# Kernel tuning notes

Hardware: AMD Instinct MI355X
Metric: run time of the kernel (lower is better)

Reference implementation:

```python
import jax, jax.numpy as jnp
import numpy as np

N, F, H, R, E = 50000, 128, 128, 8, 800000
BN_EPS = 1e-5


def setup_inputs() -> dict:
    key = jax.random.key(0)
    ks = jax.random.split(key, 10)
    g = lambda k, shp: jax.random.normal(k, shp, dtype=jnp.float32) * (1.0 / np.sqrt(shp[-2] if len(shp) > 1 else shp[-1]))
    return {
        "x": jax.random.normal(ks[0], (N, F), dtype=jnp.float32),
        "edge_index": jax.random.randint(ks[1], (2, E), 0, N, dtype=jnp.int32),
        "edge_type": jax.random.randint(ks[2], (E,), 0, R, dtype=jnp.int32),
        "W1": g(ks[3], (F, H)),
        "b1": jnp.zeros((H,), jnp.float32),
        "weight": g(ks[4], (R, H, H)),
        "root": g(ks[5], (H, H)),
        "bias_c": jnp.zeros((H,), jnp.float32),
        "gamma": jnp.ones((H,), jnp.float32),
        "beta": jnp.zeros((H,), jnp.float32),
        "W2": g(ks[6], (H, H)),
        "b2": jnp.zeros((H,), jnp.float32),
        "Wo": g(ks[7], (H, 1)),
        "bo": jnp.zeros((1,), jnp.float32),
    }


def reference(x, edge_index, edge_type, W1, b1, weight, root, bias_c, gamma, beta, W2, b2, Wo, bo):
    n = x.shape[0]
    r = weight.shape[0]
    src, dst = edge_index[0], edge_index[1]
    # segment id combining relation and destination node: equivalent to the
    # per-relation edge-mask + scatter-add loop in RGCNConv, but in one pass.
    seg = edge_type.astype(jnp.int32) * n + dst

    def conv(h):
        msg = h[src]                                            # [E, H] gather
        agg = jax.ops.segment_sum(msg, seg, num_segments=r * n)  # [R*N, H]
        agg = agg.reshape(r, n, -1)                             # [R, N, H]
        out = jnp.einsum('rnc,rco->no', agg, weight)            # per-relation matmul, summed
        return out + h @ root + bias_c

    def bn(h):
        mu = h.mean(axis=0)
        var = h.var(axis=0)  # biased var, matches torch BN training normalization
        return gamma * (h - mu) * jax.lax.rsqrt(var + BN_EPS) + beta

    h = x @ W1 + b1
    h = jax.nn.relu(bn(conv(h)))
    h = jax.nn.relu(bn(conv(h)))
    h = h @ W2 + b2
    h = h @ Wo + bo
    return jax.nn.sigmoid(h)
```

## Files before the change

### kernel.cpp

```cpp
#include <hip/hip_runtime.h>
#include <stdint.h>

typedef __bf16 bf16;
typedef __bf16 bf16x8 __attribute__((ext_vector_type(8)));
typedef float f32x4 __attribute__((ext_vector_type(4)));

__device__ __forceinline__ float bfbits2f(uint32_t lo16) {
    uint32_t b = lo16 << 16;
    float f;
    __builtin_memcpy(&f, &b, 4);
    return f;
}

__device__ __forceinline__ uint32_t pack2bf(float a, float b) {
    uint32_t lo = __builtin_bit_cast(unsigned short, (bf16)a);
    uint32_t hi = __builtin_bit_cast(unsigned short, (bf16)b);
    return lo | (hi << 16);
}

__device__ __forceinline__ void gload_lds16(const void* g, void* l) {
    __builtin_amdgcn_global_load_lds((const __attribute__((address_space(1))) void*)g,
                                     (__attribute__((address_space(3))) void*)l, 16, 0, 0);
}

__global__ void k_prep(const float* __restrict__ W1, const float* __restrict__ weight,
                       const float* __restrict__ root, const float* __restrict__ W2,
                       const float* __restrict__ b2, const float* __restrict__ Wo,
                       const float* __restrict__ bo, bf16* __restrict__ W1T,
                       bf16* __restrict__ WcatT2, float* __restrict__ qc, int R, int ldt) {
    int total = 16384 * (R + 2);
    for (int i = blockIdx.x * blockDim.x + threadIdx.x; i < total + 129; i += gridDim.x * blockDim.x) {
        if (i < 16384) {
            int f = i >> 7, h = i & 127;
            W1T[h * 128 + f] = (bf16)W1[f * 128 + h];
        } else if (i < total) {
            int j = i - 16384;
            int r = j >> 14, rem = j & 16383, c = rem >> 7, o = rem & 127;
            float v = (r < R) ? weight[(size_t)(r * 128 + c) * 128 + o] : root[c * 128 + o];
            WcatT2[(size_t)o * ldt + r * 128 + c] = (bf16)v;
        } else {
            int t = i - total;
            if (t < 128) {
                float s = 0.f;
                for (int j = 0; j < 128; j++) s += W2[t * 128 + j] * Wo[j];
                qc[t] = s;
            } else {
                float c = bo[0];
                for (int j = 0; j < 128; j++) c += b2[j] * Wo[j];
                qc[128] = c;
            }
        }
    }
}

__global__ void k_hist(const int* __restrict__ dst, const int* __restrict__ etype,
                       int* __restrict__ cnt, int E, int R) {
    for (int e = blockIdx.x * blockDim.x + threadIdx.x; e < E; e += gridDim.x * blockDim.x)
        atomicAdd(&cnt[dst[e] * R + etype[e]], 1);
}

__global__ __launch_bounds__(256) void k_scan_blk(const int* __restrict__ cnt, int* __restrict__ bsum, int M) {
    int i = blockIdx.x * 256 + threadIdx.x;
    int v = (i < M) ? cnt[i] : 0;
#pragma unroll
    for (int d = 1; d < 64; d <<= 1) v += __shfl_xor(v, d);
    __shared__ int ws[4];
    if ((threadIdx.x & 63) == 0) ws[threadIdx.x >> 6] = v;
    __syncthreads();
    if (threadIdx.x == 0) bsum[blockIdx.x] = ws[0] + ws[1] + ws[2] + ws[3];
}

__global__ __launch_bounds__(256) void k_scan_top(int* __restrict__ bsum, int nb) {
    __shared__ int s[256];
    __shared__ int carry;
    int t = threadIdx.x;
    if (t == 0) carry = 0;
    __syncthreads();
    for (int base = 0; base < nb; base += 256) {
        int i = base + t;
        int v = (i < nb) ? bsum[i] : 0;
        s[t] = v;
        __syncthreads();
#pragma unroll
        for (int d = 1; d < 256; d <<= 1) {
            int u = (t >= d) ? s[t - d] : 0;
            __syncthreads();
            s[t] += u;
            __syncthreads();
        }
        int excl = carry + s[t] - v;
        int tot = s[255];
        __syncthreads();
        if (i < nb) bsum[i] = excl;
        if (t == 0) carry += tot;
        __syncthreads();
    }
}

__global__ __launch_bounds__(256) void k_scan_apply(const int* __restrict__ cnt, const int* __restrict__ bsum,
                                                    int* __restrict__ row_off, int* __restrict__ cursor, int M) {
    int b = blockIdx.x, t = threadIdx.x;
    int i = b * 256 + t;
    int v = (i < M) ? cnt[i] : 0;
    int lane = t & 63, wid = t >> 6;
    int incl = v;
#pragma unroll
    for (int d = 1; d < 64; d <<= 1) {
        int u = __shfl_up(incl, d);
        if (lane >= d) incl += u;
    }
    __shared__ int ws[4];
    if (lane == 63) ws[wid] = incl;
    __syncthreads();
    int woff = 0;
    for (int wj = 0; wj < 4; wj++)
        if (wj < wid) woff += ws[wj];
    int excl = bsum[b] + woff + incl - v;
    if (i < M) {
        row_off[i] = excl;
        cursor[i] = excl;
        if (i == M - 1) row_off[M] = excl + v;
    }
}

__global__ void k_fill(const int* __restrict__ src, const int* __restrict__ dst,
                       const int* __restrict__ etype, int* __restrict__ cursor,
                       int* __restrict__ csr, int E, int R, int pbase) {
    int p = blockIdx.x & 7;
    int bg = blockIdx.x >> 3;
    int nchunk = gridDim.x >> 3;
    int chunk = (E + nchunk - 1) / nchunk;
    int beg = bg * chunk, end = min(beg + chunk, E);
    int lo = p * pbase, hi = lo + pbase;
    for (int e = beg + (int)threadIdx.x; e < end; e += blockDim.x) {
        int et = etype[e];
        int seg = dst[e] * R + et;
        if (seg >= lo && seg < hi) {
            int pos = atomicAdd(&cursor[seg], 1);
            csr[pos] = (et << 16) | src[e];
        }
    }
}

__global__ __launch_bounds__(256) void k_gemm0(const float* __restrict__ A, const bf16* __restrict__ BT,
                                               const float* __restrict__ bias, bf16* __restrict__ C, int M) {
    __shared__ bf16 sA[128 * 128];
    __shared__ bf16 sB[128 * 128];
    int tid = threadIdx.x;
    int m0 = blockIdx.x * 128;
#pragma unroll
    for (int i = 0; i < 8; i++) {
        int chunk = i * 256 + tid;
        int row = chunk >> 4, c16 = chunk & 15;
        int sw = ((c16 ^ (row & 7)) << 3);
        int gr = m0 + row;
        int4 va = {0, 0, 0, 0};
        if (gr < M) {
            const float* ap = A + (size_t)gr * 128 + (c16 << 3);
            float4 f0 = *reinterpret_cast<const float4*>(ap);
            float4 f1 = *reinterpret_cast<const float4*>(ap + 4);
            bf16 tmp[8] = {(bf16)f0.x, (bf16)f0.y, (bf16)f0.z, (bf16)f0.w,
                           (bf16)f1.x, (bf16)f1.y, (bf16)f1.z, (bf16)f1.w};
            __builtin_memcpy(&va, tmp, 16);
        }
        *reinterpret_cast<int4*>(&sA[row * 128 + sw]) = va;
        int4 vb = *reinterpret_cast<const int4*>(&BT[(size_t)row * 128 + (c16 << 3)]);
        *reinterpret_cast<int4*>(&sB[row * 128 + sw]) = vb;
    }
    __syncthreads();

    int lane = tid & 63, w = tid >> 6;
    int wm = (w >> 1) * 64, wn = (w & 1) * 64;
    int lr = lane & 15, lk = lane >> 4;
    f32x4 zero = {0.f, 0.f, 0.f, 0.f};
    f32x4 acc[4][4];
#pragma unroll
    for (int mi = 0; mi < 4; mi++)
#pragma unroll
        for (int ni = 0; ni < 4; ni++) acc[mi][ni] = zero;

#pragma unroll
    for (int kk = 0; kk < 4; kk++) {
        int c = (kk << 2) + lk;
        bf16x8 af[4], bfr[4];
#pragma unroll
        for (int mi = 0; mi < 4; mi++) {
            int r = wm + mi * 16 + lr;
            af[mi] = *reinterpret_cast<const bf16x8*>(&sA[r * 128 + ((c ^ (r & 7)) << 3)]);
        }
#pragma unroll
        for (int ni = 0; ni < 4; ni++) {
            int r = wn + ni * 16 + lr;
            bfr[ni] = *reinterpret_cast<const bf16x8*>(&sB[r * 128 + ((c ^ (r & 7)) << 3)]);
        }
#pragma unroll
        for (int mi = 0; mi < 4; mi++)
#pragma unroll
            for (int ni = 0; ni < 4; ni++)
                acc[mi][ni] = __builtin_amdgcn_mfma_f32_16x16x32_bf16(af[mi], bfr[ni], acc[mi][ni], 0, 0, 0);
    }

#pragma unroll
    for (int ni = 0; ni < 4; ni++) {
        int col = wn + ni * 16 + lr;
        float bia = bias[col];
#pragma unroll
        for (int mi = 0; mi < 4; mi++) {
#pragma unroll
            for (int j = 0; j < 4; j++) {
                int row = m0 + wm + mi * 16 + lk * 4 + j;
                if (row < M) C[(size_t)row * 128 + col] = (bf16)(acc[mi][ni][j] + bia);
            }
        }
    }
}

__global__ __launch_bounds__(128) void k_agg2(const bf16* __restrict__ h, const int* __restrict__ row_off,
                                              const int* __restrict__ csr, bf16* __restrict__ G, int N, int R) {
    __shared__ float acc[2][8 * 128];
    int wi = threadIdx.x >> 6;
    int n = blockIdx.x * 2 + wi;
    if (n >= N) return;
    int lane = threadIdx.x & 63;
    int c0 = lane * 2;
    float* a = acc[wi];
#pragma unroll
    for (int i = 0; i < 16; i++) a[i * 64 + lane] = 0.f;
    int beg = row_off[n * R], end = row_off[n * R + R];
    int cur = -1;
    float a0 = 0.f, a1 = 0.f;
    int i = beg;
    for (; i + 4 <= end; i += 4) {
        int p0 = csr[i], p1 = csr[i + 1], p2 = csr[i + 2], p3 = csr[i + 3];
        uint32_t v0 = *reinterpret_cast<const uint32_t*>(&h[(size_t)(p0 & 0xffff) * 128 + c0]);
        uint32_t v1 = *reinterpret_cast<const uint32_t*>(&h[(size_t)(p1 & 0xffff) * 128 + c0]);
        uint32_t v2 = *reinterpret_cast<const uint32_t*>(&h[(size_t)(p2 & 0xffff) * 128 + c0]);
        uint32_t v3 = *reinterpret_cast<const uint32_t*>(&h[(size_t)(p3 & 0xffff) * 128 + c0]);
        {
            int r = p0 >> 16; bool s = (r == cur);
            a0 = (s ? a0 : 0.f) + bfbits2f(v0 & 0xffffu);
            a1 = (s ? a1 : 0.f) + bfbits2f(v0 >> 16);
            cur = r;
            float2 st = {a0, a1};
            *reinterpret_cast<float2*>(&a[r * 128 + c0]) = st;
        }
        {
            int r = p1 >> 16; bool s = (r == cur);
            a0 = (s ? a0 : 0.f) + bfbits2f(v1 & 0xffffu);
            a1 = (s ? a1 : 0.f) + bfbits2f(v1 >> 16);
            cur = r;
            float2 st = {a0, a1};
            *reinterpret_cast<float2*>(&a[r * 128 + c0]) = st;
        }
        {
            int r = p2 >> 16; bool s = (r == cur);
            a0 = (s ? a0 : 0.f) + bfbits2f(v2 & 0xffffu);
            a1 = (s ? a1 : 0.f) + bfbits2f(v2 >> 16);
            cur = r;
            float2 st = {a0, a1};
            *reinterpret_cast<float2*>(&a[r * 128 + c0]) = st;
        }
        {
            int r = p3 >> 16; bool s = (r == cur);
            a0 = (s ? a0 : 0.f) + bfbits2f(v3 & 0xffffu);
            a1 = (s ? a1 : 0.f) + bfbits2f(v3 >> 16);
            cur = r;
            float2 st = {a0, a1};
            *reinterpret_cast<float2*>(&a[r * 128 + c0]) = st;
        }
    }
    for (; i < end; i++) {
        int p = csr[i];
        uint32_t v = *reinterpret_cast<const uint32_t*>(&h[(size_t)(p & 0xffff) * 128 + c0]);
        int r = p >> 16; bool s = (r == cur);
        a0 = (s ? a0 : 0.f) + bfbits2f(v & 0xffffu);
        a1 = (s ? a1 : 0.f) + bfbits2f(v >> 16);
        cur = r;
        float2 st = {a0, a1};
        *reinterpret_cast<float2*>(&a[r * 128 + c0]) = st;
    }
    size_t gbase = (size_t)n * 1024 + c0;
#pragma unroll
    for (int r = 0; r < 8; r++) {
        __builtin_nontemporal_store(pack2bf(a[r * 128 + c0], a[r * 128 + c0 + 1]),
                                    reinterpret_cast<uint32_t*>(&G[gbase + r * 128]));
    }
}

__global__ __launch_bounds__(256) void k_gemm2(const bf16* __restrict__ G, const bf16* __restrict__ hsrc,
                                               const bf16* __restrict__ BT, const float* __restrict__ bias,
                                               float* __restrict__ C, float* __restrict__ stats,
                                               int M, int K) {
    __shared__ bf16 sA[128 * 128];
    __shared__ bf16 sB[128 * 128];
    __shared__ float csum[128], csum2[128];
    int tid = threadIdx.x;
    if (tid < 128) { csum[tid] = 0.f; csum2[tid] = 0.f; }
    int m0 = blockIdx.x * 128;
    int lane = tid & 63, w = tid >> 6;
    int wm = (w >> 1) * 64, wn = (w & 1) * 64;
    int lr = lane & 15, lk = lane >> 4;
    int l4 = lane >> 4, c16 = lane & 15;
    f32x4 zero = {0.f, 0.f, 0.f, 0.f};
    f32x4 acc[4][4];
#pragma unroll
    for (int mi = 0; mi < 4; mi++)
#pragma unroll
        for (int ni = 0; ni < 4; ni++) acc[mi][ni] = zero;

    int KT = K >> 7;
    size_t ldg = (size_t)(K - 128);
    for (int kt = 0; kt < KT; kt++) {
        bool lastt = (kt == KT - 1);
        const bf16* Abase = lastt ? hsrc : G;
        size_t ldA = lastt ? 128 : ldg;
        int ka = lastt ? 0 : (kt << 7);
        int k0 = kt << 7;
#pragma unroll
        for (int i = 0; i < 8; i++) {
            int row = i * 16 + (w << 2) + l4;
            int cs = (c16 ^ (row & 7)) << 3;
            int gr = m0 + row;
            gr = gr < M ? gr : M - 1;
            gload_lds16(Abase + (size_t)gr * ldA + ka + cs, &sA[(i * 256 + (w << 6)) * 8]);
            gload_lds16(&BT[(size_t)row * K + k0 + cs], &sB[(i * 256 + (w << 6)) * 8]);
        }
        asm volatile("s_waitcnt vmcnt(0)" ::: "memory");
        __syncthreads();

#pragma unroll
        for (int kk = 0; kk < 4; kk++) {
            int c = (kk << 2) + lk;
            bf16x8 af[4], bfr[4];
#pragma unroll
            for (int mi = 0; mi < 4; mi++) {
                int r = wm + mi * 16 + lr;
                af[mi] = *reinterpret_cast<const bf16x8*>(&sA[r * 128 + ((c ^ (r & 7)) << 3)]);
            }
#pragma unroll
            for (int ni = 0; ni < 4; ni++) {
                int r = wn + ni * 16 + lr;
                bfr[ni] = *reinterpret_cast<const bf16x8*>(&sB[r * 128 + ((c ^ (r & 7)) << 3)]);
            }
#pragma unroll
            for (int mi = 0; mi < 4; mi++)
#pragma unroll
                for (int ni = 0; ni < 4; ni++)
                    acc[mi][ni] = __builtin_amdgcn_mfma_f32_16x16x32_bf16(af[mi], bfr[ni], acc[mi][ni], 0, 0, 0);
        }
        __syncthreads();
    }

    float ls[4], ls2[4];
#pragma unroll
    for (int ni = 0; ni < 4; ni++) { ls[ni] = 0.f; ls2[ni] = 0.f; }
#pragma unroll
    for (int ni = 0; ni < 4; ni++) {
        int col = wn + ni * 16 + lr;
        float bia = bias[col];
#pragma unroll
        for (int mi = 0; mi < 4; mi++) {
#pragma unroll
            for (int j = 0; j < 4; j++) {
                int row = m0 + wm + mi * 16 + lk * 4 + j;
                if (row < M) {
                    float val = acc[mi][ni][j] + bia;
                    C[(size_t)row * 128 + col] = val;
                    ls[ni] += val;
                    ls2[ni] += val * val;
                }
            }
        }
    }
#pragma unroll
    for (int ni = 0; ni < 4; ni++) {
        float s = ls[ni], s2 = ls2[ni];
        s += __shfl_xor(s, 16); s += __shfl_xor(s, 32);
        s2 += __shfl_xor(s2, 16); s2 += __shfl_xor(s2, 32);
        if (lk == 0) {
            int col = wn + ni * 16 + lr;
            atomicAdd(&csum[col], s);
            atomicAdd(&csum2[col], s2);
        }
    }
    __syncthreads();
    if (tid < 128) {
        atomicAdd(&stats[tid], csum[tid]);
        atomicAdd(&stats[128 + tid], csum2[tid]);
    }
}

__global__ void k_bnfin(float* __restrict__ stats, const float* __restrict__ gamma,
                        const float* __restrict__ beta, float* __restrict__ bnp, float invN) {
    int t = threadIdx.x;
    float mu = stats[t] * invN;
    float var = stats[128 + t] * invN - mu * mu;
    float sc = gamma[t] * rsqrtf(var + 1e-5f);
    bnp[t] = sc;
    bnp[128 + t] = beta[t] - mu * sc;
    stats[t] = 0.f;
    stats[128 + t] = 0.f;
}

__global__ void k_bnrelu(const float* __restrict__ conv, const float* __restrict__ bnp,
                         bf16* __restrict__ h, int N) {
    int total = N * 32;
    for (int i = blockIdx.x * blockDim.x + threadIdx.x; i < total; i += gridDim.x * blockDim.x) {
        int c4 = (i & 31) << 2;
        float4 v = *reinterpret_cast<const float4*>(&conv[(size_t)i * 4]);
        const float* vv = &v.x;
        uint64_t pk = 0;
#pragma unroll
        for (int j = 0; j < 4; j++) {
            int c = c4 + j;
            float val = fmaxf(vv[j] * bnp[c] + bnp[128 + c], 0.f);
            unsigned short us = __builtin_bit_cast(unsigned short, (bf16)val);
            pk |= (uint64_t)us << (16 * j);
        }
        *reinterpret_cast<uint64_t*>(&h[(size_t)i * 4]) = pk;
    }
}

__global__ __launch_bounds__(256) void k_bnout(const float* __restrict__ conv, const float* __restrict__ bnp,
                                               const float* __restrict__ qc, float* __restrict__ out, int N) {
    int wi = threadIdx.x >> 6;
    int n = blockIdx.x * 4 + wi;
    if (n >= N) return;
    int lane = threadIdx.x & 63;
    int c0 = lane * 2;
    float2 v = *reinterpret_cast<const float2*>(&conv[(size_t)n * 128 + c0]);
    float v0 = fmaxf(v.x * bnp[c0] + bnp[128 + c0], 0.f);
    float v1 = fmaxf(v.y * bnp[c0 + 1] + bnp[128 + c0 + 1], 0.f);
    float s = v0 * qc[c0] + v1 * qc[c0 + 1];
#pragma unroll
    for (int d = 1; d < 64; d <<= 1) s += __shfl_xor(s, d);
    if (lane == 0) out[n] = 1.f / (1.f + expf(-(s + qc[128])));
}

extern "C" void kernel_launch(void* const* d_in, const int* in_sizes, int n_in,
                              void* d_out, int out_size, void* d_ws, size_t ws_size,
                              hipStream_t stream) {
    const float* x      = (const float*)d_in[0];
    const int*   ei     = (const int*)d_in[1];
    const int*   etype  = (const int*)d_in[2];
    const float* W1     = (const float*)d_in[3];
    const float* b1     = (const float*)d_in[4];
    const float* weight = (const float*)d_in[5];
    const float* root   = (const float*)d_in[6];
    const float* bias_c = (const float*)d_in[7];
    const float* gamma  = (const float*)d_in[8];
    const float* beta   = (const float*)d_in[9];
    const float* W2     = (const float*)d_in[10];
    const float* b2     = (const float*)d_in[11];
    const float* Wo     = (const float*)d_in[12];
    const float* bo     = (const float*)d_in[13];
    float* out = (float*)d_out;

    int H = in_sizes[4];
    int F = in_sizes[3] / H;
    int N = in_sizes[0] / F;
    int E = in_sizes[2];
    int R = in_sizes[5] / (H * H);
    int ldt = (R + 1) * H;
    int M = N * R;

    const int* srcv = ei;
    const int* dstv = ei + E;

    char* p = (char*)d_ws;
    auto alloc = [&](size_t bytes) -> char* {
        char* r = p;
        p += (bytes + 255) & ~(size_t)255;
        return r;
    };
    bf16*  G       = (bf16*)alloc((size_t)N * (R * H) * 2);
    bf16*  h       = (bf16*)alloc((size_t)N * H * 2);
    float* conv    = (float*)alloc((size_t)N * H * 4);
    bf16*  WcatT2  = (bf16*)alloc((size_t)ldt * H * 2);
    bf16*  W1T     = (bf16*)alloc((size_t)F * H * 2);
    float* qc      = (float*)alloc(129 * 4);
    int*   cnt     = (int*)alloc((size_t)M * 4);
    int*   row_off = (int*)alloc((size_t)(M + 1) * 4);
    int*   cursor  = (int*)alloc((size_t)M * 4);
    int*   csr     = (int*)alloc((size_t)E * 4);
    float* stats   = (float*)alloc(256 * 4);
    float* bnp     = (float*)alloc(256 * 4);
    int*   bsum    = (int*)alloc(2048 * 4);
    if ((size_t)(p - (char*)d_ws) > ws_size) return;

    int nb = (M + 255) / 256;
    int pbase = (M + 7) / 8;

    hipMemsetAsync(cnt, 0, (size_t)M * 4, stream);
    hipMemsetAsync(stats, 0, 256 * 4, stream);
    k_prep<<<256, 256, 0, stream>>>(W1, weight, root, W2, b2, Wo, bo, W1T, WcatT2, qc, R, ldt);
    k_hist<<<1024, 256, 0, stream>>>(dstv, etype, cnt, E, R);
    k_scan_blk<<<nb, 256, 0, stream>>>(cnt, bsum, M);
    k_scan_top<<<1, 256, 0, stream>>>(bsum, nb);
    k_scan_apply<<<nb, 256, 0, stream>>>(cnt, bsum, row_off, cursor, M);
    k_fill<<<1024, 256, 0, stream>>>(srcv, dstv, etype, cursor, csr, E, R, pbase);

    int mb = (N + 127) / 128;
    k_gemm0<<<mb, 256, 0, stream>>>(x, W1T, b1, h, N);

    for (int l = 0; l < 2; l++) {
        k_agg2<<<(N + 1) / 2, 128, 0, stream>>>(h, row_off, csr, G, N, R);
        k_gemm2<<<mb, 256, 0, stream>>>(G, h, WcatT2, bias_c, conv, stats, N, ldt);
        k_bnfin<<<1, 128, 0, stream>>>(stats, gamma, beta, bnp, 1.f / (float)N);
        if (l == 0)
            k_bnrelu<<<2048, 256, 0, stream>>>(conv, bnp, h, N);
        else
            k_bnout<<<(N + 3) / 4, 256, 0, stream>>>(conv, bnp, qc, out, N);
    }
}
```

Baseline: 304.0 us.

## Read GEMM weights directly from global memory and fold BN finalize into consumers

```diff
diff --git a/kernel.cpp b/kernel.cpp
--- a/kernel.cpp
+++ b/kernel.cpp
@@ -292,7 +292,6 @@
                                                float* __restrict__ C, float* __restrict__ stats,
                                                int M, int K) {
     __shared__ bf16 sA[128 * 128];
-    __shared__ bf16 sB[128 * 128];
     __shared__ float csum[128], csum2[128];
     int tid = threadIdx.x;
     if (tid < 128) { csum[tid] = 0.f; csum2[tid] = 0.f; }
@@ -323,7 +322,6 @@
             int gr = m0 + row;
             gr = gr < M ? gr : M - 1;
             gload_lds16(Abase + (size_t)gr * ldA + ka + cs, &sA[(i * 256 + (w << 6)) * 8]);
-            gload_lds16(&BT[(size_t)row * K + k0 + cs], &sB[(i * 256 + (w << 6)) * 8]);
         }
         asm volatile("s_waitcnt vmcnt(0)" ::: "memory");
         __syncthreads();
@@ -339,8 +337,8 @@
             }
 #pragma unroll
             for (int ni = 0; ni < 4; ni++) {
-                int r = wn + ni * 16 + lr;
-                bfr[ni] = *reinterpret_cast<const bf16x8*>(&sB[r * 128 + ((c ^ (r & 7)) << 3)]);
+                int o = wn + ni * 16 + lr;
+                bfr[ni] = *reinterpret_cast<const bf16x8*>(&BT[(size_t)o * K + k0 + (c << 3)]);
             }
 #pragma unroll
             for (int mi = 0; mi < 4; mi++)
@@ -390,20 +388,9 @@
     }
 }
 
-__global__ void k_bnfin(float* __restrict__ stats, const float* __restrict__ gamma,
-                        const float* __restrict__ beta, float* __restrict__ bnp, float invN) {
-    int t = threadIdx.x;
-    float mu = stats[t] * invN;
-    float var = stats[128 + t] * invN - mu * mu;
-    float sc = gamma[t] * rsqrtf(var + 1e-5f);
-    bnp[t] = sc;
-    bnp[128 + t] = beta[t] - mu * sc;
-    stats[t] = 0.f;
-    stats[128 + t] = 0.f;
-}
-
-__global__ void k_bnrelu(const float* __restrict__ conv, const float* __restrict__ bnp,
-                         bf16* __restrict__ h, int N) {
+__global__ void k_bnrelu(const float* __restrict__ conv, const float* __restrict__ stats,
+                         const float* __restrict__ gamma, const float* __restrict__ beta,
+                         bf16* __restrict__ h, int N, float invN) {
     int total = N * 32;
     for (int i = blockIdx.x * blockDim.x + threadIdx.x; i < total; i += gridDim.x * blockDim.x) {
         int c4 = (i & 31) << 2;
@@ -413,7 +400,11 @@
 #pragma unroll
         for (int j = 0; j < 4; j++) {
             int c = c4 + j;
-            float val = fmaxf(vv[j] * bnp[c] + bnp[128 + c], 0.f);
+            float mu = stats[c] * invN;
+            float var = stats[128 + c] * invN - mu * mu;
+            float sc = gamma[c] * rsqrtf(var + 1e-5f);
+            float sh = beta[c] - mu * sc;
+            float val = fmaxf(vv[j] * sc + sh, 0.f);
             unsigned short us = __builtin_bit_cast(unsigned short, (bf16)val);
             pk |= (uint64_t)us << (16 * j);
         }
@@ -421,16 +412,26 @@
     }
 }
 
-__global__ __launch_bounds__(256) void k_bnout(const float* __restrict__ conv, const float* __restrict__ bnp,
-                                               const float* __restrict__ qc, float* __restrict__ out, int N) {
+__global__ __launch_bounds__(256) void k_bnout(const float* __restrict__ conv, const float* __restrict__ stats,
+                                               const float* __restrict__ gamma, const float* __restrict__ beta,
+                                               const float* __restrict__ qc, float* __restrict__ out,
+                                               int N, float invN) {
     int wi = threadIdx.x >> 6;
     int n = blockIdx.x * 4 + wi;
     if (n >= N) return;
     int lane = threadIdx.x & 63;
     int c0 = lane * 2;
+    float mu0 = stats[c0] * invN;
+    float var0 = stats[128 + c0] * invN - mu0 * mu0;
+    float sc0 = gamma[c0] * rsqrtf(var0 + 1e-5f);
+    float sh0 = beta[c0] - mu0 * sc0;
+    float mu1 = stats[c0 + 1] * invN;
+    float var1 = stats[128 + c0 + 1] * invN - mu1 * mu1;
+    float sc1 = gamma[c0 + 1] * rsqrtf(var1 + 1e-5f);
+    float sh1 = beta[c0 + 1] - mu1 * sc1;
     float2 v = *reinterpret_cast<const float2*>(&conv[(size_t)n * 128 + c0]);
-    float v0 = fmaxf(v.x * bnp[c0] + bnp[128 + c0], 0.f);
-    float v1 = fmaxf(v.y * bnp[c0 + 1] + bnp[128 + c0 + 1], 0.f);
+    float v0 = fmaxf(v.x * sc0 + sh0, 0.f);
+    float v1 = fmaxf(v.y * sc1 + sh1, 0.f);
     float s = v0 * qc[c0] + v1 * qc[c0 + 1];
 #pragma unroll
     for (int d = 1; d < 64; d <<= 1) s += __shfl_xor(s, d);
@@ -483,8 +484,7 @@
     int*   row_off = (int*)alloc((size_t)(M + 1) * 4);
     int*   cursor  = (int*)alloc((size_t)M * 4);
     int*   csr     = (int*)alloc((size_t)E * 4);
-    float* stats   = (float*)alloc(256 * 4);
-    float* bnp     = (float*)alloc(256 * 4);
+    float* stats   = (float*)alloc(512 * 4);
     int*   bsum    = (int*)alloc(2048 * 4);
     if ((size_t)(p - (char*)d_ws) > ws_size) return;
 
@@ -492,7 +492,7 @@
     int pbase = (M + 7) / 8;
 
     hipMemsetAsync(cnt, 0, (size_t)M * 4, stream);
-    hipMemsetAsync(stats, 0, 256 * 4, stream);
+    hipMemsetAsync(stats, 0, 512 * 4, stream);
     k_prep<<<256, 256, 0, stream>>>(W1, weight, root, W2, b2, Wo, bo, W1T, WcatT2, qc, R, ldt);
     k_hist<<<1024, 256, 0, stream>>>(dstv, etype, cnt, E, R);
     k_scan_blk<<<nb, 256, 0, stream>>>(cnt, bsum, M);
@@ -503,13 +503,14 @@
     int mb = (N + 127) / 128;
     k_gemm0<<<mb, 256, 0, stream>>>(x, W1T, b1, h, N);
 
+    float invN = 1.f / (float)N;
     for (int l = 0; l < 2; l++) {
+        float* statsl = stats + l * 256;
         k_agg2<<<(N + 1) / 2, 128, 0, stream>>>(h, row_off, csr, G, N, R);
-        k_gemm2<<<mb, 256, 0, stream>>>(G, h, WcatT2, bias_c, conv, stats, N, ldt);
-        k_bnfin<<<1, 128, 0, stream>>>(stats, gamma, beta, bnp, 1.f / (float)N);
+        k_gemm2<<<mb, 256, 0, stream>>>(G, h, WcatT2, bias_c, conv, statsl, N, ldt);
         if (l == 0)
-            k_bnrelu<<<2048, 256, 0, stream>>>(conv, bnp, h, N);
+            k_bnrelu<<<2048, 256, 0, stream>>>(conv, statsl, gamma, beta, h, N, invN);
         else
-            k_bnout<<<(N + 3) / 4, 256, 0, stream>>>(conv, bnp, qc, out, N);
-    }
-}
+            k_bnout<<<(N + 3) / 4, 256, 0, stream>>>(conv, statsl, gamma, beta, qc, out, N, invN);
+    }
+}
```

After: 343.3 us. 12.9% more time.
